# Performance work log

Hardware: AMD Instinct MI355X
Metric: run time of the kernel (lower is better)

The kernel has to match this reference:

```python
import jax, jax.numpy as jnp
import numpy as np

N = 100000      # nodes
E = 3200000     # edges
F_IN = 512
HID = 16
C = 10


def setup_inputs() -> dict:
    key = jax.random.key(0)
    k1, k2, k3, k4 = jax.random.split(key, 4)
    x = jax.random.normal(k1, (N, F_IN), dtype=jnp.float32)
    edge_index = jax.random.randint(k2, (2, E), 0, N, dtype=jnp.int64)
    W1 = jax.random.normal(k3, (F_IN, HID), dtype=jnp.float32) * 0.05
    b1 = jnp.zeros((HID,), dtype=jnp.float32)
    W2 = jax.random.normal(k4, (HID, C), dtype=jnp.float32) * 0.05
    b2 = jnp.zeros((C,), dtype=jnp.float32)
    return {"x": x, "edge_index": edge_index, "W1": W1, "b1": b1, "W2": W2, "b2": b2}


def _gcn_norm(edge_index, n):
    # add self-loops, compute symmetric normalization deg^-1/2 * deg^-1/2
    loops = jnp.arange(n, dtype=edge_index.dtype)
    src = jnp.concatenate([edge_index[0], loops])
    dst = jnp.concatenate([edge_index[1], loops])
    deg = jax.ops.segment_sum(jnp.ones_like(dst, dtype=jnp.float32), dst, num_segments=n)
    dinv = jnp.where(deg > 0, jax.lax.rsqrt(deg), 0.0)
    norm = dinv[src] * dinv[dst]  # [E+N]
    return src, dst, norm


def _gcn_layer(h, W, b, src, dst, norm, n):
    h = h @ W                                   # project first (PyG GCNConv)
    msg = h[src] * norm[:, None]                # gather + edge scaling
    agg = jax.ops.segment_sum(msg, dst, num_segments=n)  # scatter-add
    return agg + b


def reference(x, edge_index, W1, b1, W2, b2):
    n = x.shape[0]
    src, dst, norm = _gcn_norm(edge_index, n)
    h = jax.nn.relu(_gcn_layer(x, W1, b1, src, dst, norm, n))
    # F.dropout with training=False is identity (eval mode)
    out = _gcn_layer(h, W2, b2, src, dst, norm, n)
    return jax.nn.log_softmax(out, axis=1)
```

## Files before the change

### kernel.cpp

```cpp
#include <hip/hip_runtime.h>
#include <hip/hip_fp16.h>

#define N_NODES 100000
#define N_EDGES 3200000
#define F_IN    512
#define HID     16
#define NCLS    10
#define NB      196
#define EPB     4096
#define TK      32

union H2F { __half2 h; float f; };
__device__ __forceinline__ float h2f_pack(float a, float b) {
    H2F u; u.h = __floats2half2_rn(a, b); return u.f;
}
__device__ __forceinline__ void h2f_add(float raw, float& a, float& b) {
    H2F u; u.f = raw; float2 v = __half22float2(u.h); a += v.x; b += v.y;
}
__device__ __forceinline__ void acc4(float2 raw, float& a, float& b, float& c, float& d) {
    h2f_add(raw.x, a, b); h2f_add(raw.y, c, d);
}

__global__ __launch_bounds__(256) void k_bhist(const int4* __restrict__ dst4,
                                               int* __restrict__ bcntp) {
    __shared__ int h[256];
    int t = threadIdx.x;
    h[t] = 0;
    __syncthreads();
    int base4 = blockIdx.x * 2048;
    int hi4 = min(N_EDGES / 4, base4 + 2048);
    for (int e4 = base4 + t; e4 < hi4; e4 += 256) {
        int4 d = dst4[e4];
        atomicAdd(&h[d.x >> 9], 1);
        atomicAdd(&h[d.y >> 9], 1);
        atomicAdd(&h[d.z >> 9], 1);
        atomicAdd(&h[d.w >> 9], 1);
    }
    __syncthreads();
    if (t < NB) {
        int v = h[t];
        if (v) atomicAdd(&bcntp[t * 16], v);
    }
}

__global__ __launch_bounds__(256) void k_bscan(const int* __restrict__ bcntp,
                                               int* __restrict__ boff,
                                               int* __restrict__ bcurp,
                                               int* __restrict__ row) {
    __shared__ int sh[256];
    int t = threadIdx.x;
    int v = (t < NB) ? bcntp[t * 16] : 0;
    sh[t] = v;
    __syncthreads();
    for (int off = 1; off < 256; off <<= 1) {
        int add = (t >= off) ? sh[t - off] : 0;
        __syncthreads();
        sh[t] += add;
        __syncthreads();
    }
    int excl = sh[t] - v;
    if (t < NB) { boff[t] = excl; bcurp[t * 16] = excl; }
    if (t == 0) { boff[NB] = N_EDGES; row[N_NODES] = N_EDGES; }
}

__global__ __launch_bounds__(256) void k_bpart(const int* __restrict__ ei,
                                               int* __restrict__ bcurp,
                                               int* __restrict__ part) {
    __shared__ int cnt_sh[256], base_sh[256];
    int t = threadIdx.x;
    cnt_sh[t] = 0;
    __syncthreads();
    const int4* s4 = (const int4*)ei;
    const int4* d4 = (const int4*)(ei + N_EDGES);
    int base4 = blockIdx.x * 1024;
    int pk[16], bk[16], rk[16];
#pragma unroll
    for (int j = 0; j < 4; ++j) {
        int e4 = base4 + j * 256 + t;
        if (e4 < N_EDGES / 4) {
            int4 s = s4[e4], d = d4[e4];
            bk[4 * j + 0] = d.x >> 9; pk[4 * j + 0] = ((d.x & 511) << 17) | s.x;
            bk[4 * j + 1] = d.y >> 9; pk[4 * j + 1] = ((d.y & 511) << 17) | s.y;
            bk[4 * j + 2] = d.z >> 9; pk[4 * j + 2] = ((d.z & 511) << 17) | s.z;
            bk[4 * j + 3] = d.w >> 9; pk[4 * j + 3] = ((d.w & 511) << 17) | s.w;
            rk[4 * j + 0] = atomicAdd(&cnt_sh[bk[4 * j + 0]], 1);
            rk[4 * j + 1] = atomicAdd(&cnt_sh[bk[4 * j + 1]], 1);
            rk[4 * j + 2] = atomicAdd(&cnt_sh[bk[4 * j + 2]], 1);
            rk[4 * j + 3] = atomicAdd(&cnt_sh[bk[4 * j + 3]], 1);
        } else {
            bk[4 * j + 0] = -1; bk[4 * j + 1] = -1;
            bk[4 * j + 2] = -1; bk[4 * j + 3] = -1;
        }
    }
    __syncthreads();
    if (t < NB && cnt_sh[t] > 0)
        base_sh[t] = atomicAdd(&bcurp[t * 16], cnt_sh[t]);
    __syncthreads();
#pragma unroll
    for (int j = 0; j < 16; ++j)
        if (bk[j] >= 0) part[base_sh[bk[j]] + rk[j]] = pk[j];
}

__global__ __launch_bounds__(1024) void k_bucket(const int* __restrict__ boff,
                                                 const int* __restrict__ part,
                                                 int* __restrict__ row,
                                                 float* __restrict__ dinv,
                                                 int* __restrict__ srcs) {
    __shared__ int cnt[512], ofs[512];
    int t = threadIdx.x;
    int b = blockIdx.x;
    int e0 = boff[b], e1 = boff[b + 1];
    int nbase = b << 9;
    if (t < 512) cnt[t] = 0;
    __syncthreads();
    for (int e = e0 + t; e < e1; e += 4096) {
        int p0 = part[e];
        int p1 = (e + 1024 < e1) ? part[e + 1024] : -1;
        int p2 = (e + 2048 < e1) ? part[e + 2048] : -1;
        int p3 = (e + 3072 < e1) ? part[e + 3072] : -1;
        atomicAdd(&cnt[p0 >> 17], 1);
        if (p1 >= 0) atomicAdd(&cnt[p1 >> 17], 1);
        if (p2 >= 0) atomicAdd(&cnt[p2 >> 17], 1);
        if (p3 >= 0) atomicAdd(&cnt[p3 >> 17], 1);
    }
    __syncthreads();
    int v = (t < 512) ? cnt[t] : 0;
    if (t < 512) ofs[t] = v;
    __syncthreads();
    for (int off = 1; off < 512; off <<= 1) {
        int add = (t >= off && t < 512) ? ofs[t - off] : 0;
        __syncthreads();
        if (t < 512) ofs[t] += add;
        __syncthreads();
    }
    int excl = (t < 512) ? (ofs[t] - v) : 0;
    __syncthreads();
    if (t < 512) {
        ofs[t] = excl;
        int n = nbase + t;
        if (n < N_NODES) {
            row[n] = e0 + excl;
            dinv[n] = rsqrtf((float)(v + 1));
        }
    }
    __syncthreads();
    for (int e = e0 + t; e < e1; e += 4096) {
        int p0 = part[e];
        int p1 = (e + 1024 < e1) ? part[e + 1024] : -1;
        int p2 = (e + 2048 < e1) ? part[e + 2048] : -1;
        int p3 = (e + 3072 < e1) ? part[e + 3072] : -1;
        int o0 = atomicAdd(&ofs[p0 >> 17], 1);
        srcs[e0 + o0] = p0 & 0x1FFFF;
        if (p1 >= 0) { int o = atomicAdd(&ofs[p1 >> 17], 1); srcs[e0 + o] = p1 & 0x1FFFF; }
        if (p2 >= 0) { int o = atomicAdd(&ofs[p2 >> 17], 1); srcs[e0 + o] = p2 & 0x1FFFF; }
        if (p3 >= 0) { int o = atomicAdd(&ofs[p3 >> 17], 1); srcs[e0 + o] = p3 & 0x1FFFF; }
    }
}

__global__ __launch_bounds__(128) void k_gemm1(const float* __restrict__ x,
                                               const float* __restrict__ W1,
                                               const float* __restrict__ dinv,
                                               __half* __restrict__ h1h) {
    __shared__ float xs[256][TK + 1];
    __shared__ float wchunk[TK * 16];
    const int t = threadIdx.x;
    const int nbase = blockIdx.x * 256;
    const int f4 = t & 7;
    const int r0 = t >> 3;

    float4 pre[16];
#pragma unroll
    for (int p = 0; p < 16; ++p) {
        int n = nbase + r0 + p * 16;
        pre[p] = (n < N_NODES) ? ((const float4*)(x + (size_t)n * F_IN))[f4]
                               : make_float4(0.f, 0.f, 0.f, 0.f);
    }
    float4 wpre = ((const float4*)W1)[t];

    float acc0[16], acc1[16];
#pragma unroll
    for (int j = 0; j < 16; ++j) { acc0[j] = 0.f; acc1[j] = 0.f; }

    for (int c = 0; c < F_IN; c += TK) {
#pragma unroll
        for (int p = 0; p < 16; ++p) {
            int r = r0 + p * 16;
            xs[r][f4 * 4 + 0] = pre[p].x;
            xs[r][f4 * 4 + 1] = pre[p].y;
            xs[r][f4 * 4 + 2] = pre[p].z;
            xs[r][f4 * 4 + 3] = pre[p].w;
        }
        ((float4*)wchunk)[t] = wpre;
        __syncthreads();
        if (c + TK < F_IN) {
#pragma unroll
            for (int p = 0; p < 16; ++p) {
                int n = nbase + r0 + p * 16;
                pre[p] = (n < N_NODES)
                           ? ((const float4*)(x + (size_t)n * F_IN + c + TK))[f4]
                           : make_float4(0.f, 0.f, 0.f, 0.f);
            }
            wpre = ((const float4*)(W1 + (c + TK) * 16))[t];
        }
#pragma unroll
        for (int k = 0; k < TK; ++k) {
            float xv0 = xs[t][k];
            float xv1 = xs[t + 128][k];
            const float4* wk = (const float4*)&wchunk[k * 16];
            float4 wa = wk[0], wb = wk[1], wc = wk[2], wd = wk[3];
            acc0[0]  = fmaf(xv0, wa.x, acc0[0]);   acc1[0]  = fmaf(xv1, wa.x, acc1[0]);
            acc0[1]  = fmaf(xv0, wa.y, acc0[1]);   acc1[1]  = fmaf(xv1, wa.y, acc1[1]);
            acc0[2]  = fmaf(xv0, wa.z, acc0[2]);   acc1[2]  = fmaf(xv1, wa.z, acc1[2]);
            acc0[3]  = fmaf(xv0, wa.w, acc0[3]);   acc1[3]  = fmaf(xv1, wa.w, acc1[3]);
            acc0[4]  = fmaf(xv0, wb.x, acc0[4]);   acc1[4]  = fmaf(xv1, wb.x, acc1[4]);
            acc0[5]  = fmaf(xv0, wb.y, acc0[5]);   acc1[5]  = fmaf(xv1, wb.y, acc1[5]);
            acc0[6]  = fmaf(xv0, wb.z, acc0[6]);   acc1[6]  = fmaf(xv1, wb.z, acc1[6]);
            acc0[7]  = fmaf(xv0, wb.w, acc0[7]);   acc1[7]  = fmaf(xv1, wb.w, acc1[7]);
            acc0[8]  = fmaf(xv0, wc.x, acc0[8]);   acc1[8]  = fmaf(xv1, wc.x, acc1[8]);
            acc0[9]  = fmaf(xv0, wc.y, acc0[9]);   acc1[9]  = fmaf(xv1, wc.y, acc1[9]);
            acc0[10] = fmaf(xv0, wc.z, acc0[10]);  acc1[10] = fmaf(xv1, wc.z, acc1[10]);
            acc0[11] = fmaf(xv0, wc.w, acc0[11]);  acc1[11] = fmaf(xv1, wc.w, acc1[11]);
            acc0[12] = fmaf(xv0, wd.x, acc0[12]);  acc1[12] = fmaf(xv1, wd.x, acc1[12]);
            acc0[13] = fmaf(xv0, wd.y, acc0[13]);  acc1[13] = fmaf(xv1, wd.y, acc1[13]);
            acc0[14] = fmaf(xv0, wd.z, acc0[14]);  acc1[14] = fmaf(xv1, wd.z, acc1[14]);
            acc0[15] = fmaf(xv0, wd.w, acc0[15]);  acc1[15] = fmaf(xv1, wd.w, acc1[15]);
        }
        __syncthreads();
    }

    int n0 = nbase + t;
    if (n0 < N_NODES) {
        float dn = dinv[n0];
        float4 o0 = make_float4(h2f_pack(acc0[0]  * dn, acc0[1]  * dn),
                                h2f_pack(acc0[2]  * dn, acc0[3]  * dn),
                                h2f_pack(acc0[4]  * dn, acc0[5]  * dn),
                                h2f_pack(acc0[6]  * dn, acc0[7]  * dn));
        float4 o1 = make_float4(h2f_pack(acc0[8]  * dn, acc0[9]  * dn),
                                h2f_pack(acc0[10] * dn, acc0[11] * dn),
                                h2f_pack(acc0[12] * dn, acc0[13] * dn),
                                h2f_pack(acc0[14] * dn, acc0[15] * dn));
        float4* o = (float4*)(h1h + (size_t)n0 * 16);
        o[0] = o0; o[1] = o1;
    }
    int n1 = nbase + 128 + t;
    if (n1 < N_NODES) {
        float dn = dinv[n1];
        float4 o0 = make_float4(h2f_pack(acc1[0]  * dn, acc1[1]  * dn),
                                h2f_pack(acc1[2]  * dn, acc1[3]  * dn),
                                h2f_pack(acc1[4]  * dn, acc1[5]  * dn),
                                h2f_pack(acc1[6]  * dn, acc1[7]  * dn));
        float4 o1 = make_float4(h2f_pack(acc1[8]  * dn, acc1[9]  * dn),
                                h2f_pack(acc1[10] * dn, acc1[11] * dn),
                                h2f_pack(acc1[12] * dn, acc1[13] * dn),
                                h2f_pack(acc1[14] * dn, acc1[15] * dn));
        float4* o = (float4*)(h1h + (size_t)n1 * 16);
        o[0] = o0; o[1] = o1;
    }
}

__global__ __launch_bounds__(256) void k_edge1f(const int* __restrict__ row,
                                                const int* __restrict__ srcs,
                                                const float* __restrict__ dinv,
                                                const __half* __restrict__ h1h,
                                                const float* __restrict__ b1,
                                                const float* __restrict__ W2,
                                                __half* __restrict__ ps) {
    __shared__ float w2s[HID * NCLS];
    if (threadIdx.x < HID * NCLS) w2s[threadIdx.x] = W2[threadIdx.x];
    __syncthreads();
    int t = blockIdx.x * 256 + threadIdx.x;
    if (t >= N_NODES * 4) return;
    int n = t >> 2, q = t & 3;
    const float2* h2 = (const float2*)h1h;
    float s0 = 0.f, s1 = 0.f, s2 = 0.f, s3 = 0.f;
    acc4(h2[n * 4 + q], s0, s1, s2, s3);
    int k = row[n], k1 = row[n + 1];
    for (; k + 16 <= k1; k += 16) {
        int a[16];
#pragma unroll
        for (int j = 0; j < 16; ++j) a[j] = srcs[k + j];
        float2 v[16];
#pragma unroll
        for (int j = 0; j < 16; ++j) v[j] = h2[a[j] * 4 + q];
#pragma unroll
        for (int j = 0; j < 16; ++j) acc4(v[j], s0, s1, s2, s3);
    }
    if (k < k1) {
        int sb = srcs[k];
        int a[16];
#pragma unroll
        for (int j = 0; j < 16; ++j) a[j] = (k + j < k1) ? srcs[k + j] : sb;
        float2 v[16];
#pragma unroll
        for (int j = 0; j < 16; ++j) v[j] = h2[a[j] * 4 + q];
#pragma unroll
        for (int j = 0; j < 16; ++j)
            if (k + j < k1) acc4(v[j], s0, s1, s2, s3);
    }
    float dn = dinv[n];
    int c0 = q * 4;
    float r0 = fmaxf(fmaf(dn, s0, b1[c0 + 0]), 0.f);
    float r1 = fmaxf(fmaf(dn, s1, b1[c0 + 1]), 0.f);
    float r2 = fmaxf(fmaf(dn, s2, b1[c0 + 2]), 0.f);
    float r3 = fmaxf(fmaf(dn, s3, b1[c0 + 3]), 0.f);
    float p[NCLS];
#pragma unroll
    for (int c = 0; c < NCLS; ++c)
        p[c] = r0 * w2s[(c0 + 0) * NCLS + c] + r1 * w2s[(c0 + 1) * NCLS + c]
             + r2 * w2s[(c0 + 2) * NCLS + c] + r3 * w2s[(c0 + 3) * NCLS + c];
#pragma unroll
    for (int c = 0; c < NCLS; ++c) {
        p[c] += __shfl_xor(p[c], 1);
        p[c] += __shfl_xor(p[c], 2);
    }
    float o0, o1, o2, o3;
    if (q == 0)      { o0 = p[0]; o1 = p[1]; o2 = p[2]; o3 = p[3]; }
    else if (q == 1) { o0 = p[4]; o1 = p[5]; o2 = p[6]; o3 = p[7]; }
    else if (q == 2) { o0 = p[8]; o1 = p[9]; o2 = 0.f;  o3 = 0.f;  }
    else             { o0 = 0.f;  o1 = 0.f;  o2 = 0.f;  o3 = 0.f;  }
    float2 st = make_float2(h2f_pack(o0 * dn, o1 * dn), h2f_pack(o2 * dn, o3 * dn));
    ((float2*)ps)[n * 4 + q] = st;
}

__global__ __launch_bounds__(256) void k_edge2f(const int* __restrict__ row,
                                                const int* __restrict__ srcs,
                                                const float* __restrict__ dinv,
                                                const __half* __restrict__ ps,
                                                const float* __restrict__ b2,
                                                float* __restrict__ out) {
    int t = blockIdx.x * 256 + threadIdx.x;
    if (t >= N_NODES * 4) return;
    int n = t >> 2, q = t & 3;
    const float2* p2 = (const float2*)ps;
    float s0 = 0.f, s1 = 0.f, s2 = 0.f, s3 = 0.f;
    acc4(p2[n * 4 + q], s0, s1, s2, s3);
    int k = row[n], k1 = row[n + 1];
    for (; k + 16 <= k1; k += 16) {
        int a[16];
#pragma unroll
        for (int j = 0; j < 16; ++j) a[j] = srcs[k + j];
        float2 v[16];
#pragma unroll
        for (int j = 0; j < 16; ++j) v[j] = p2[a[j] * 4 + q];
#pragma unroll
        for (int j = 0; j < 16; ++j) acc4(v[j], s0, s1, s2, s3);
    }
    if (k < k1) {
        int sb = srcs[k];
        int a[16];
#pragma unroll
        for (int j = 0; j < 16; ++j) a[j] = (k + j < k1) ? srcs[k + j] : sb;
        float2 v[16];
#pragma unroll
        for (int j = 0; j < 16; ++j) v[j] = p2[a[j] * 4 + q];
#pragma unroll
        for (int j = 0; j < 16; ++j)
            if (k + j < k1) acc4(v[j], s0, s1, s2, s3);
    }
    float dn = dinv[n];
    int c0 = q * 4;
    float v0 = (c0 + 0 < NCLS) ? fmaf(dn, s0, b2[c0 + 0]) : -1e30f;
    float v1 = (c0 + 1 < NCLS) ? fmaf(dn, s1, b2[c0 + 1]) : -1e30f;
    float v2 = (c0 + 2 < NCLS) ? fmaf(dn, s2, b2[c0 + 2]) : -1e30f;
    float v3 = (c0 + 3 < NCLS) ? fmaf(dn, s3, b2[c0 + 3]) : -1e30f;
    float m = fmaxf(fmaxf(v0, v1), fmaxf(v2, v3));
    m = fmaxf(m, __shfl_xor(m, 1));
    m = fmaxf(m, __shfl_xor(m, 2));
    float se = __expf(v0 - m) + __expf(v1 - m) + __expf(v2 - m) + __expf(v3 - m);
    se += __shfl_xor(se, 1);
    se += __shfl_xor(se, 2);
    float l = m + __logf(se);
    if (q < 2) {
        float* o = out + n * NCLS + c0;
        o[0] = v0 - l; o[1] = v1 - l; o[2] = v2 - l; o[3] = v3 - l;
    } else if (q == 2) {
        float* o = out + n * NCLS + 8;
        o[0] = v0 - l; o[1] = v1 - l;
    }
}

extern "C" void kernel_launch(void* const* d_in, const int* in_sizes, int n_in,
                              void* d_out, int out_size, void* d_ws, size_t ws_size,
                              hipStream_t stream) {
    const float* x  = (const float*)d_in[0];
    const int*   ei = (const int*)d_in[1];
    const float* W1 = (const float*)d_in[2];
    const float* b1 = (const float*)d_in[3];
    const float* W2 = (const float*)d_in[4];
    const float* b2 = (const float*)d_in[5];
    float* out = (float*)d_out;

    int* w = (int*)d_ws;
    float*  dinv  = (float*)w;
    int*    row   = w + 102400;
    int*    bcntp = w + 204816;
    int*    bcurp = w + 207952;
    int*    boff  = w + 211088;
    int*    part  = w + 211344;
    int*    srcs  = w + 3411344;
    __half* h1h   = (__half*)(w + 6611344);
    __half* ps    = (__half*)(w + 9888144);

    hipMemsetAsync(bcntp, 0, NB * 16 * sizeof(int), stream);
    k_bhist<<<(N_EDGES + 8191) / 8192, 256, 0, stream>>>((const int4*)(ei + N_EDGES), bcntp);
    k_bscan<<<1, 256, 0, stream>>>(bcntp, boff, bcurp, row);
    k_bpart<<<(N_EDGES + EPB - 1) / EPB, 256, 0, stream>>>(ei, bcurp, part);
    k_bucket<<<NB, 1024, 0, stream>>>(boff, part, row, dinv, srcs);

    k_gemm1 <<<(N_NODES + 255) / 256, 128, 0, stream>>>(x, W1, dinv, h1h);
    k_edge1f<<<(N_NODES * 4 + 255) / 256, 256, 0, stream>>>(row, srcs, dinv, h1h, b1, W2, ps);
    k_edge2f<<<(N_NODES * 4 + 255) / 256, 256, 0, stream>>>(row, srcs, dinv, ps, b2, out);
}
```

Before: 436.6 us.

## Use two threads per node with 16-byte gathers and compact layer-2 rows

The first aggregation kernel now uses two threads per node, each gathering a 16-byte float4 (8 half features) instead of four threads gathering 8 bytes each. This halves the number of index loads and gather instructions per edge. The intermediate layer-2 projection is stored as 12 halves per node (24 bytes) instead of 16 (32 bytes), which shrinks the gather footprint for the second aggregation. The fourth lane in the second kernel now duplicates lane 2's loads and is masked out of the softmax sum, so it still spends bandwidth, and 24-byte rows may straddle cache lines.

```diff
diff --git a/kernel.cpp b/kernel.cpp
--- a/kernel.cpp
+++ b/kernel.cpp
@@ -19,6 +19,11 @@
 }
 __device__ __forceinline__ void acc4(float2 raw, float& a, float& b, float& c, float& d) {
     h2f_add(raw.x, a, b); h2f_add(raw.y, c, d);
+}
+__device__ __forceinline__ void acc8(float4 raw, float& a0, float& a1, float& a2, float& a3,
+                                     float& a4, float& a5, float& a6, float& a7) {
+    h2f_add(raw.x, a0, a1); h2f_add(raw.y, a2, a3);
+    h2f_add(raw.z, a4, a5); h2f_add(raw.w, a6, a7);
 }
 
 __global__ __launch_bounds__(256) void k_bhist(const int4* __restrict__ dst4,
@@ -258,7 +263,7 @@
     }
 }
 
-__global__ __launch_bounds__(256) void k_edge1f(const int* __restrict__ row,
+__global__ __launch_bounds__(512) void k_edge1p(const int* __restrict__ row,
                                                 const int* __restrict__ srcs,
                                                 const float* __restrict__ dinv,
                                                 const __half* __restrict__ h1h,
@@ -268,58 +273,69 @@
     __shared__ float w2s[HID * NCLS];
     if (threadIdx.x < HID * NCLS) w2s[threadIdx.x] = W2[threadIdx.x];
     __syncthreads();
-    int t = blockIdx.x * 256 + threadIdx.x;
-    if (t >= N_NODES * 4) return;
-    int n = t >> 2, q = t & 3;
-    const float2* h2 = (const float2*)h1h;
-    float s0 = 0.f, s1 = 0.f, s2 = 0.f, s3 = 0.f;
-    acc4(h2[n * 4 + q], s0, s1, s2, s3);
+    int t = blockIdx.x * 512 + threadIdx.x;
+    if (t >= N_NODES * 2) return;
+    int n = t >> 1, p = t & 1;
+    const float4* h4 = (const float4*)h1h;
+    float s[8];
+#pragma unroll
+    for (int j = 0; j < 8; ++j) s[j] = 0.f;
+    acc8(h4[n * 2 + p], s[0], s[1], s[2], s[3], s[4], s[5], s[6], s[7]);
     int k = row[n], k1 = row[n + 1];
     for (; k + 16 <= k1; k += 16) {
         int a[16];
 #pragma unroll
         for (int j = 0; j < 16; ++j) a[j] = srcs[k + j];
-        float2 v[16];
-#pragma unroll
-        for (int j = 0; j < 16; ++j) v[j] = h2[a[j] * 4 + q];
-#pragma unroll
-        for (int j = 0; j < 16; ++j) acc4(v[j], s0, s1, s2, s3);
+        float4 v[16];
+#pragma unroll
+        for (int j = 0; j < 16; ++j) v[j] = h4[a[j] * 2 + p];
+#pragma unroll
+        for (int j = 0; j < 16; ++j)
+            acc8(v[j], s[0], s[1], s[2], s[3], s[4], s[5], s[6], s[7]);
     }
     if (k < k1) {
         int sb = srcs[k];
         int a[16];
 #pragma unroll
         for (int j = 0; j < 16; ++j) a[j] = (k + j < k1) ? srcs[k + j] : sb;
-        float2 v[16];
-#pragma unroll
-        for (int j = 0; j < 16; ++j) v[j] = h2[a[j] * 4 + q];
+        float4 v[16];
+#pragma unroll
+        for (int j = 0; j < 16; ++j) v[j] = h4[a[j] * 2 + p];
 #pragma unroll
         for (int j = 0; j < 16; ++j)
-            if (k + j < k1) acc4(v[j], s0, s1, s2, s3);
+            if (k + j < k1)
+                acc8(v[j], s[0], s[1], s[2], s[3], s[4], s[5], s[6], s[7]);
     }
     float dn = dinv[n];
-    int c0 = q * 4;
-    float r0 = fmaxf(fmaf(dn, s0, b1[c0 + 0]), 0.f);
-    float r1 = fmaxf(fmaf(dn, s1, b1[c0 + 1]), 0.f);
-    float r2 = fmaxf(fmaf(dn, s2, b1[c0 + 2]), 0.f);
-    float r3 = fmaxf(fmaf(dn, s3, b1[c0 + 3]), 0.f);
-    float p[NCLS];
+    int c0 = p * 8;
+    float r[8];
+#pragma unroll
+    for (int j = 0; j < 8; ++j)
+        r[j] = fmaxf(fmaf(dn, s[j], b1[c0 + j]), 0.f);
+    float pc[NCLS];
+#pragma unroll
+    for (int c = 0; c < NCLS; ++c) {
+        float acc = 0.f;
+#pragma unroll
+        for (int j = 0; j < 8; ++j)
+            acc = fmaf(r[j], w2s[(c0 + j) * NCLS + c], acc);
+        pc[c] = acc;
+    }
 #pragma unroll
     for (int c = 0; c < NCLS; ++c)
-        p[c] = r0 * w2s[(c0 + 0) * NCLS + c] + r1 * w2s[(c0 + 1) * NCLS + c]
-             + r2 * w2s[(c0 + 2) * NCLS + c] + r3 * w2s[(c0 + 3) * NCLS + c];
-#pragma unroll
-    for (int c = 0; c < NCLS; ++c) {
-        p[c] += __shfl_xor(p[c], 1);
-        p[c] += __shfl_xor(p[c], 2);
-    }
-    float o0, o1, o2, o3;
-    if (q == 0)      { o0 = p[0]; o1 = p[1]; o2 = p[2]; o3 = p[3]; }
-    else if (q == 1) { o0 = p[4]; o1 = p[5]; o2 = p[6]; o3 = p[7]; }
-    else if (q == 2) { o0 = p[8]; o1 = p[9]; o2 = 0.f;  o3 = 0.f;  }
-    else             { o0 = 0.f;  o1 = 0.f;  o2 = 0.f;  o3 = 0.f;  }
-    float2 st = make_float2(h2f_pack(o0 * dn, o1 * dn), h2f_pack(o2 * dn, o3 * dn));
-    ((float2*)ps)[n * 4 + q] = st;
+        pc[c] += __shfl_xor(pc[c], 1);
+    if (p == 0) {
+        float2 st0 = make_float2(h2f_pack(pc[0] * dn, pc[1] * dn),
+                                 h2f_pack(pc[2] * dn, pc[3] * dn));
+        ((float2*)ps)[n * 3 + 0] = st0;
+        float2 st2 = make_float2(h2f_pack(pc[8] * dn, pc[9] * dn),
+                                 h2f_pack(0.f, 0.f));
+        ((float2*)ps)[n * 3 + 2] = st2;
+    } else {
+        float2 st1 = make_float2(h2f_pack(pc[4] * dn, pc[5] * dn),
+                                 h2f_pack(pc[6] * dn, pc[7] * dn));
+        ((float2*)ps)[n * 3 + 1] = st1;
+    }
 }
 
 __global__ __launch_bounds__(256) void k_edge2f(const int* __restrict__ row,
@@ -331,9 +347,10 @@
     int t = blockIdx.x * 256 + threadIdx.x;
     if (t >= N_NODES * 4) return;
     int n = t >> 2, q = t & 3;
+    int qc = (q < 3) ? q : 2;
     const float2* p2 = (const float2*)ps;
     float s0 = 0.f, s1 = 0.f, s2 = 0.f, s3 = 0.f;
-    acc4(p2[n * 4 + q], s0, s1, s2, s3);
+    acc4(p2[n * 3 + qc], s0, s1, s2, s3);
     int k = row[n], k1 = row[n + 1];
     for (; k + 16 <= k1; k += 16) {
         int a[16];
@@ -341,7 +358,7 @@
         for (int j = 0; j < 16; ++j) a[j] = srcs[k + j];
         float2 v[16];
 #pragma unroll
-        for (int j = 0; j < 16; ++j) v[j] = p2[a[j] * 4 + q];
+        for (int j = 0; j < 16; ++j) v[j] = p2[a[j] * 3 + qc];
 #pragma unroll
         for (int j = 0; j < 16; ++j) acc4(v[j], s0, s1, s2, s3);
     }
@@ -352,21 +369,22 @@
         for (int j = 0; j < 16; ++j) a[j] = (k + j < k1) ? srcs[k + j] : sb;
         float2 v[16];
 #pragma unroll
-        for (int j = 0; j < 16; ++j) v[j] = p2[a[j] * 4 + q];
+        for (int j = 0; j < 16; ++j) v[j] = p2[a[j] * 3 + qc];
 #pragma unroll
         for (int j = 0; j < 16; ++j)
             if (k + j < k1) acc4(v[j], s0, s1, s2, s3);
     }
     float dn = dinv[n];
-    int c0 = q * 4;
-    float v0 = (c0 + 0 < NCLS) ? fmaf(dn, s0, b2[c0 + 0]) : -1e30f;
-    float v1 = (c0 + 1 < NCLS) ? fmaf(dn, s1, b2[c0 + 1]) : -1e30f;
+    int c0 = qc * 4;
+    float v0 = fmaf(dn, s0, b2[c0 + 0]);
+    float v1 = fmaf(dn, s1, b2[c0 + 1]);
     float v2 = (c0 + 2 < NCLS) ? fmaf(dn, s2, b2[c0 + 2]) : -1e30f;
     float v3 = (c0 + 3 < NCLS) ? fmaf(dn, s3, b2[c0 + 3]) : -1e30f;
     float m = fmaxf(fmaxf(v0, v1), fmaxf(v2, v3));
     m = fmaxf(m, __shfl_xor(m, 1));
     m = fmaxf(m, __shfl_xor(m, 2));
     float se = __expf(v0 - m) + __expf(v1 - m) + __expf(v2 - m) + __expf(v3 - m);
+    if (q == 3) se = 0.f;
     se += __shfl_xor(se, 1);
     se += __shfl_xor(se, 2);
     float l = m + __logf(se);
@@ -408,6 +426,6 @@
     k_bucket<<<NB, 1024, 0, stream>>>(boff, part, row, dinv, srcs);
 
     k_gemm1 <<<(N_NODES + 255) / 256, 128, 0, stream>>>(x, W1, dinv, h1h);
-    k_edge1f<<<(N_NODES * 4 + 255) / 256, 256, 0, stream>>>(row, srcs, dinv, h1h, b1, W2, ps);
+    k_edge1p<<<(N_NODES * 2 + 511) / 512, 512, 0, stream>>>(row, srcs, dinv, h1h, b1, W2, ps);
     k_edge2f<<<(N_NODES * 4 + 255) / 256, 256, 0, stream>>>(row, srcs, dinv, ps, b2, out);
 }
```

Measured after the change: 439.8 us. Within noise of the previous version (+0.7%).
